# Optimization experiments

Hardware: AMD Instinct MI355X
Metric: run time of the kernel (lower is better)

Reference implementation:

```python
import jax, jax.numpy as jnp
import numpy as np

N_NODES = 500_000
N_FEAT = 16
HIDDEN = 32
N_EDGES = 8_000_000


def setup_inputs() -> dict:
    key = jax.random.key(0)
    ks = jax.random.split(key, 12)
    x = jax.random.normal(ks[0], (N_NODES, N_FEAT), dtype=jnp.float32)
    edge_index = jax.random.randint(ks[1], (2, N_EDGES), 0, N_NODES, dtype=jnp.int32)
    edge_weight = jax.random.uniform(ks[2], (N_EDGES,), dtype=jnp.float32)
    h = 0.1 * jax.random.normal(ks[3], (N_NODES, HIDDEN), dtype=jnp.float32)
    c = 0.1 * jax.random.normal(ks[4], (N_NODES, HIDDEN), dtype=jnp.float32)
    s = 0.1  # glorot-ish scale
    # Gate order along axis 0: (i, f, c~, o). K=1 ChebConv == Linear.
    W_x = s * jax.random.normal(ks[5], (4, N_FEAT, HIDDEN), dtype=jnp.float32)
    b_x = s * jax.random.normal(ks[6], (4, HIDDEN), dtype=jnp.float32)
    W_h = s * jax.random.normal(ks[7], (4, HIDDEN, HIDDEN), dtype=jnp.float32)
    b_h = s * jax.random.normal(ks[8], (4, HIDDEN), dtype=jnp.float32)
    w_c = s * jax.random.normal(ks[9], (3, HIDDEN), dtype=jnp.float32)  # peephole (i, f, o)
    b_g = s * jax.random.normal(ks[10], (4, HIDDEN), dtype=jnp.float32)  # per-gate bias b_i,b_f,b_c,b_o
    W_lin = s * jax.random.normal(ks[11], (HIDDEN, 1), dtype=jnp.float32)
    b_lin = jnp.zeros((1,), dtype=jnp.float32)
    return {"x": x, "edge_index": edge_index, "edge_weight": edge_weight,
            "h": h, "c": c, "W_x": W_x, "b_x": b_x, "W_h": W_h, "b_h": b_h,
            "w_c": w_c, "b_g": b_g, "W_lin": W_lin, "b_lin": b_lin}


def reference(x, edge_index, edge_weight, h, c, W_x, b_x, W_h, b_h, w_c, b_g, W_lin, b_lin):
    # GConvLSTM with K=1: each ChebConv degenerates to a single linear map
    # (Tx_0 = x, out = x @ W_0 + b); edge_index / edge_weight are unused by the math.
    # gx, gh: [4, N, H] — stacked (i, f, c~, o) gate pre-activations.
    gx = jnp.einsum('nf,gfh->gnh', x, W_x) + b_x[:, None, :]
    gh = jnp.einsum('nh,gho->gno', h, W_h) + b_h[:, None, :]
    s = gx + gh
    i = jax.nn.sigmoid(s[0] + w_c[0] * c + b_g[0])
    f = jax.nn.sigmoid(s[1] + w_c[1] * c + b_g[1])
    t = jnp.tanh(s[2] + b_g[2])
    c_new = f * c + i * t
    o = jax.nn.sigmoid(s[3] + w_c[2] * c_new + b_g[3])
    h0 = o * jnp.tanh(c_new)
    out = jax.nn.relu(h0) @ W_lin + b_lin  # [N, 1]
    return (out, h0, c_new)
```

## Files before the change

kernel.cpp:

```cpp
#include <hip/hip_runtime.h>
#include <hip/hip_bf16.h>

#define NF 16
#define NH 32
#define LOG2E  1.44269504088896340736f
#define TILE_NODES 32

#define T_WORDS 2560
#define XW 0
#define HW 512
#define CW 1536
#define HOUT 0
#define COUT 1152

typedef short bf16x8 __attribute__((ext_vector_type(8)));
typedef float f32x16 __attribute__((ext_vector_type(16)));
typedef float f32x4  __attribute__((ext_vector_type(4)));

#if __has_builtin(__builtin_amdgcn_exp2f)
#define EXP2(x) __builtin_amdgcn_exp2f(x)
#else
#define EXP2(x) exp2f(x)
#endif

__device__ __forceinline__ short f2bf(float f) {
    __hip_bfloat16 b = __float2bfloat16(f);
    return *reinterpret_cast<short*>(&b);
}

__device__ __forceinline__ bf16x8 cvt8(float4 a, float4 b) {
    bf16x8 r;
    r[0] = f2bf(a.x); r[1] = f2bf(a.y); r[2] = f2bf(a.z); r[3] = f2bf(a.w);
    r[4] = f2bf(b.x); r[5] = f2bf(b.y); r[6] = f2bf(b.z); r[7] = f2bf(b.w);
    return r;
}

__device__ __forceinline__ float sig2(float v) {
    return __builtin_amdgcn_rcpf(1.0f + EXP2(-v));
}
__device__ __forceinline__ float tanh2(float v) {
    return 1.0f - 2.0f * __builtin_amdgcn_rcpf(1.0f + EXP2(v));
}

__device__ __forceinline__ void gload_lds16(const float* g, float* l) {
    __builtin_amdgcn_global_load_lds(
        (const __attribute__((address_space(1))) void*)g,
        (__attribute__((address_space(3))) void*)l, 16, 0, 0);
}

__device__ __forceinline__ void nt_store4(float* p, float4 v) {
    f32x4 w = { v.x, v.y, v.z, v.w };
    __builtin_nontemporal_store(w, (f32x4*)p);
}

struct Frags { bf16x8 w[4][4]; bf16x8 a3; };

__global__ void prep_kernel(const float* __restrict__ Wx, const float* __restrict__ Wh,
                            const float* __restrict__ bx, const float* __restrict__ bh,
                            const float* __restrict__ bg, const float* __restrict__ wc,
                            short* __restrict__ Wpack, float* __restrict__ wcs)
{
    int t = blockIdx.x * blockDim.x + threadIdx.x;
    if (t < 4 * 4 * 64) {
        int g  = t >> 8;
        int ks = (t >> 6) & 3;
        int l  = t & 63;
        int col  = l & 31;
        int half = l >> 5;
        float scale = (g == 2) ? 2.0f * LOG2E : LOG2E;
        #pragma unroll
        for (int e = 0; e < 8; ++e) {
            int gk = ks * 16 + half * 8 + e;
            float w;
            if (gk < NF)            w = Wx[(g * NF + gk) * NH + col];
            else if (gk < NF + NH)  w = Wh[(g * NH + (gk - NF)) * NH + col];
            else if (gk == 48)      w = bx[g * NH + col] + bh[g * NH + col] + bg[g * NH + col];
            else                    w = 0.0f;
            Wpack[t * 8 + e] = f2bf(w * scale);
        }
    }
    if (t < 3 * NH) wcs[t] = wc[t] * LOG2E;
}

__device__ __forceinline__ void prefetch_tile(const float* __restrict__ x,
                                              const float* __restrict__ hin,
                                              const float* __restrict__ cin,
                                              long nb, float* ws,
                                              const int* xoff, const int* hoff)
{
    asm volatile("" ::: "memory");
    const float* xb = x   + nb * NF;
    const float* hb = hin + nb * NH;
    const float* cb = cin + nb * NH;
    #pragma unroll
    for (int i = 0; i < 2; ++i) gload_lds16(xb + xoff[i], ws + XW + i * 256);
    #pragma unroll
    for (int i = 0; i < 4; ++i) gload_lds16(hb + hoff[i], ws + HW + i * 256);
    #pragma unroll
    for (int i = 0; i < 4; ++i) gload_lds16(cb + hoff[i], ws + CW + i * 256);
    asm volatile("" ::: "memory");
}

__device__ __forceinline__ void do_tile(float* ws, long nb, const Frags& F,
                                        const float* __restrict__ wcs,
                                        const float* __restrict__ Wlin, float bl,
                                        float* __restrict__ out,
                                        float* __restrict__ h0o,
                                        float* __restrict__ co, int lane)
{
    const int col  = lane & 31;
    const int half = lane >> 5;
    const int c3 = col & 3, c7 = col & 7;

    float4 x0 = *(const float4*)&ws[XW + (col * 4 + ((2 * half)     ^ c3)) * 4];
    float4 x1 = *(const float4*)&ws[XW + (col * 4 + ((2 * half + 1) ^ c3)) * 4];
    float4 h0 = *(const float4*)&ws[HW + (col * 8 + ((2 * half)     ^ c7)) * 4];
    float4 h1 = *(const float4*)&ws[HW + (col * 8 + ((2 * half + 1) ^ c7)) * 4];
    float4 h2 = *(const float4*)&ws[HW + (col * 8 + ((4 + 2 * half) ^ c7)) * 4];
    float4 h3 = *(const float4*)&ws[HW + (col * 8 + ((5 + 2 * half) ^ c7)) * 4];
    bf16x8 a0 = cvt8(x0, x1), a1 = cvt8(h0, h1), a2 = cvt8(h2, h3);

    float4 cv4[4];
    #pragma unroll
    for (int jg = 0; jg < 4; ++jg)
        cv4[jg] = *(const float4*)&ws[CW + (col * 8 + ((2 * jg + half) ^ c7)) * 4];

    f32x16 acc[4];
    #pragma unroll
    for (int g = 0; g < 4; ++g) {
        #pragma unroll
        for (int r = 0; r < 16; ++r) acc[g][r] = 0.0f;
        acc[g] = __builtin_amdgcn_mfma_f32_32x32x16_bf16(F.w[g][0], a0,   acc[g], 0, 0, 0);
        acc[g] = __builtin_amdgcn_mfma_f32_32x32x16_bf16(F.w[g][1], a1,   acc[g], 0, 0, 0);
        acc[g] = __builtin_amdgcn_mfma_f32_32x32x16_bf16(F.w[g][2], a2,   acc[g], 0, 0, 0);
        acc[g] = __builtin_amdgcn_mfma_f32_32x32x16_bf16(F.w[g][3], F.a3, acc[g], 0, 0, 0);
    }

    float outacc = 0.0f;
    const float c2l = 2.0f * LOG2E;
    #pragma unroll
    for (int jg = 0; jg < 4; ++jg) {
        const int jbase = jg * 8 + 4 * half;
        const float4 w0 = *(const float4*)(wcs + 0 * NH + jbase);
        const float4 w1 = *(const float4*)(wcs + 1 * NH + jbase);
        const float4 w2 = *(const float4*)(wcs + 2 * NH + jbase);
        const float4 wl = *(const float4*)(Wlin + jbase);
        float h4[4], c4[4];
        #pragma unroll
        for (int q = 0; q < 4; ++q) {
            const int r = jg * 4 + q;
            const float ci = ((const float*)&cv4[jg])[q];
            const float ig = sig2(fmaf(((const float*)&w0)[q], ci, acc[0][r]));
            const float fg = sig2(fmaf(((const float*)&w1)[q], ci, acc[1][r]));
            const float tg = tanh2(acc[2][r]);
            const float cn = fg * ci + ig * tg;
            const float og = sig2(fmaf(((const float*)&w2)[q], cn, acc[3][r]));
            const float hh = og * tanh2(cn * c2l);
            c4[q] = cn;
            h4[q] = hh;
            outacc = fmaf(fmaxf(hh, 0.0f), ((const float*)&wl)[q], outacc);
        }
        *(float4*)&ws[HOUT + col * 36 + jbase] = make_float4(h4[0], h4[1], h4[2], h4[3]);
        *(float4*)&ws[COUT + col * 36 + jbase] = make_float4(c4[0], c4[1], c4[2], c4[3]);
    }

    float* hrow = h0o + nb * NH;
    float* crow = co  + nb * NH;
    #pragma unroll
    for (int rep = 0; rep < 4; ++rep) {
        const int tt = lane + rep * 64;
        const int nd = tt >> 3, j4 = (tt & 7) * 4;
        float4 vh = *(const float4*)&ws[HOUT + nd * 36 + j4];
        float4 vc = *(const float4*)&ws[COUT + nd * 36 + j4];
        nt_store4(hrow + tt * 4, vh);
        nt_store4(crow + tt * 4, vc);
    }

    outacc += __shfl_xor(outacc, 32, 64);
    if (half == 0) __builtin_nontemporal_store(outacc + bl, &out[nb + col]);
}

__global__ __launch_bounds__(256, 2) void lstm_pipe_kernel(
    const float* __restrict__ x, const float* __restrict__ hin,
    const float* __restrict__ cin,
    const float* __restrict__ Wlin, const float* __restrict__ blin,
    const short* __restrict__ Wpack, const float* __restrict__ wcs,
    float* __restrict__ out, float* __restrict__ h0o, float* __restrict__ co,
    int ntiles, int wstride)
{
    __shared__ float bufA[4][T_WORDS];
    __shared__ float bufB[4][T_WORDS];

    const int lane = threadIdx.x & 63;
    const int wave = threadIdx.x >> 6;
    float* cur = bufA[wave];
    float* oth = bufB[wave];

    Frags F;
    #pragma unroll
    for (int g = 0; g < 4; ++g)
        #pragma unroll
        for (int ks = 0; ks < 4; ++ks)
            F.w[g][ks] = *(const bf16x8*)(Wpack + (((g * 4) + ks) * 64 + lane) * 8);
    #pragma unroll
    for (int e = 0; e < 8; ++e) F.a3[e] = 0;
    if ((lane >> 5) == 0) F.a3[0] = (short)0x3F80;
    const float bl = blin[0];

    int xoff[2], hoff[4];
    #pragma unroll
    for (int i = 0; i < 2; ++i) {
        int u = i * 64 + lane;
        xoff[i] = ((u & ~3) | ((u & 3) ^ ((u >> 2) & 3))) * 4;
    }
    #pragma unroll
    for (int i = 0; i < 4; ++i) {
        int u = i * 64 + lane;
        hoff[i] = ((u & ~7) | ((u & 7) ^ ((u >> 3) & 7))) * 4;
    }

    const int S = wstride;
    const int last = ntiles - 1;
    int t = blockIdx.x * 4 + wave;

    prefetch_tile(x, hin, cin, (long)t * TILE_NODES, cur, xoff, hoff);
    {
        int t1 = t + S; if (t1 > last) t1 = last;
        prefetch_tile(x, hin, cin, (long)t1 * TILE_NODES, oth, xoff, hoff);
    }

    bool first = true;
    for (;;) {
        if (first) { asm volatile("s_waitcnt vmcnt(10)" ::: "memory"); first = false; }
        else       { asm volatile("s_waitcnt vmcnt(19)" ::: "memory"); }

        do_tile(cur, (long)t * TILE_NODES, F, wcs, Wlin, bl, out, h0o, co, lane);

        int tn = t + 2 * S; if (tn > last) tn = last;
        prefetch_tile(x, hin, cin, (long)tn * TILE_NODES, cur, xoff, hoff);

        t += S;
        if (t >= ntiles) break;
        float* tmp = cur; cur = oth; oth = tmp;
    }
}

extern "C" void kernel_launch(void* const* d_in, const int* in_sizes, int n_in,
                              void* d_out, int out_size, void* d_ws, size_t ws_size,
                              hipStream_t stream) {
    const float* x    = (const float*)d_in[0];
    const float* h    = (const float*)d_in[3];
    const float* c    = (const float*)d_in[4];
    const float* Wx   = (const float*)d_in[5];
    const float* bx   = (const float*)d_in[6];
    const float* Wh   = (const float*)d_in[7];
    const float* bh   = (const float*)d_in[8];
    const float* wc   = (const float*)d_in[9];
    const float* bg   = (const float*)d_in[10];
    const float* Wlin = (const float*)d_in[11];
    const float* blin = (const float*)d_in[12];

    const int N = in_sizes[0] / NF;
    const int ntiles = N / TILE_NODES;

    float* out = (float*)d_out;
    float* h0o = out + N;
    float* co  = h0o + (size_t)N * NH;

    short* Wpack = (short*)d_ws;
    float* wcs   = (float*)((char*)d_ws + 4 * 4 * 64 * 8 * sizeof(short));

    prep_kernel<<<4, 256, 0, stream>>>(Wx, Wh, bx, bh, bg, wc, Wpack, wcs);

    const int grid = 512;
    const int wstride = grid * 4;
    lstm_pipe_kernel<<<grid, 256, 0, stream>>>(
        x, h, c, Wlin, blin, Wpack, wcs, out, h0o, co, ntiles, wstride);
}
```

Baseline: 58.18 us.

## Load cell state directly into registers and shrink LDS staging per wave

```diff
diff --git a/kernel.cpp b/kernel.cpp
--- a/kernel.cpp
+++ b/kernel.cpp
@@ -6,12 +6,11 @@
 #define LOG2E  1.44269504088896340736f
 #define TILE_NODES 32
 
-#define T_WORDS 2560
+#define IN_WORDS 1536
 #define XW 0
 #define HW 512
-#define CW 1536
-#define HOUT 0
-#define COUT 1152
+#define OSTG 33
+#define OSTG_WORDS (32 * OSTG)
 
 typedef short bf16x8 __attribute__((ext_vector_type(8)));
 typedef float f32x16 __attribute__((ext_vector_type(16)));
@@ -82,26 +81,29 @@
     if (t < 3 * NH) wcs[t] = wc[t] * LOG2E;
 }
 
-__device__ __forceinline__ void prefetch_tile(const float* __restrict__ x,
-                                              const float* __restrict__ hin,
-                                              const float* __restrict__ cin,
-                                              long nb, float* ws,
-                                              const int* xoff, const int* hoff)
+__device__ __forceinline__ void prefetch_in(const float* __restrict__ x,
+                                            const float* __restrict__ hin,
+                                            long nb, float* ws,
+                                            const int* xoff, const int* hoff)
 {
     asm volatile("" ::: "memory");
     const float* xb = x   + nb * NF;
     const float* hb = hin + nb * NH;
-    const float* cb = cin + nb * NH;
     #pragma unroll
     for (int i = 0; i < 2; ++i) gload_lds16(xb + xoff[i], ws + XW + i * 256);
     #pragma unroll
     for (int i = 0; i < 4; ++i) gload_lds16(hb + hoff[i], ws + HW + i * 256);
-    #pragma unroll
-    for (int i = 0; i < 4; ++i) gload_lds16(cb + hoff[i], ws + CW + i * 256);
     asm volatile("" ::: "memory");
 }
 
-__device__ __forceinline__ void do_tile(float* ws, long nb, const Frags& F,
+#define LOAD_C(cr, nb_) {                                                   \
+    const float* pc = cin + ((nb_) + col) * NH + 4 * half;                  \
+    cr[0] = *(const float4*)(pc);      cr[1] = *(const float4*)(pc + 8);    \
+    cr[2] = *(const float4*)(pc + 16); cr[3] = *(const float4*)(pc + 24);   \
+    asm volatile("" ::: "memory"); }
+
+__device__ __forceinline__ void do_tile(const float* ws, float* og, long nb,
+                                        const float4* cr, const Frags& F,
                                         const float* __restrict__ wcs,
                                         const float* __restrict__ Wlin, float bl,
                                         float* __restrict__ out,
@@ -120,11 +122,6 @@
     float4 h3 = *(const float4*)&ws[HW + (col * 8 + ((5 + 2 * half) ^ c7)) * 4];
     bf16x8 a0 = cvt8(x0, x1), a1 = cvt8(h0, h1), a2 = cvt8(h2, h3);
 
-    float4 cv4[4];
-    #pragma unroll
-    for (int jg = 0; jg < 4; ++jg)
-        cv4[jg] = *(const float4*)&ws[CW + (col * 8 + ((2 * jg + half) ^ c7)) * 4];
-
     f32x16 acc[4];
     #pragma unroll
     for (int g = 0; g < 4; ++g) {
@@ -138,6 +135,7 @@
 
     float outacc = 0.0f;
     const float c2l = 2.0f * LOG2E;
+    float c4s0[4], c4s1[4], c4s2[4], c4s3[4];
     #pragma unroll
     for (int jg = 0; jg < 4; ++jg) {
         const int jbase = jg * 8 + 4 * half;
@@ -145,36 +143,51 @@
         const float4 w1 = *(const float4*)(wcs + 1 * NH + jbase);
         const float4 w2 = *(const float4*)(wcs + 2 * NH + jbase);
         const float4 wl = *(const float4*)(Wlin + jbase);
-        float h4[4], c4[4];
+        float h4[4];
         #pragma unroll
         for (int q = 0; q < 4; ++q) {
             const int r = jg * 4 + q;
-            const float ci = ((const float*)&cv4[jg])[q];
+            const float ci = ((const float*)&cr[jg])[q];
             const float ig = sig2(fmaf(((const float*)&w0)[q], ci, acc[0][r]));
             const float fg = sig2(fmaf(((const float*)&w1)[q], ci, acc[1][r]));
             const float tg = tanh2(acc[2][r]);
             const float cn = fg * ci + ig * tg;
-            const float og = sig2(fmaf(((const float*)&w2)[q], cn, acc[3][r]));
-            const float hh = og * tanh2(cn * c2l);
-            c4[q] = cn;
+            const float og_ = sig2(fmaf(((const float*)&w2)[q], cn, acc[3][r]));
+            const float hh = og_ * tanh2(cn * c2l);
+            if (jg == 0) c4s0[q] = cn; else if (jg == 1) c4s1[q] = cn;
+            else if (jg == 2) c4s2[q] = cn; else c4s3[q] = cn;
             h4[q] = hh;
             outacc = fmaf(fmaxf(hh, 0.0f), ((const float*)&wl)[q], outacc);
         }
-        *(float4*)&ws[HOUT + col * 36 + jbase] = make_float4(h4[0], h4[1], h4[2], h4[3]);
-        *(float4*)&ws[COUT + col * 36 + jbase] = make_float4(c4[0], c4[1], c4[2], c4[3]);
+        *(float4*)&og[col * OSTG + jbase] = make_float4(h4[0], h4[1], h4[2], h4[3]);
     }
 
     float* hrow = h0o + nb * NH;
     float* crow = co  + nb * NH;
+    float4 vh[4];
     #pragma unroll
     for (int rep = 0; rep < 4; ++rep) {
         const int tt = lane + rep * 64;
-        const int nd = tt >> 3, j4 = (tt & 7) * 4;
-        float4 vh = *(const float4*)&ws[HOUT + nd * 36 + j4];
-        float4 vc = *(const float4*)&ws[COUT + nd * 36 + j4];
-        nt_store4(hrow + tt * 4, vh);
-        nt_store4(crow + tt * 4, vc);
-    }
+        vh[rep] = *(const float4*)&og[(tt >> 3) * OSTG + (tt & 7) * 4];
+    }
+    #pragma unroll
+    for (int rep = 0; rep < 4; ++rep) nt_store4(hrow + (lane + rep * 64) * 4, vh[rep]);
+
+    {
+        const int jb0 = 4 * half;
+        *(float4*)&og[col * OSTG + jb0]      = make_float4(c4s0[0], c4s0[1], c4s0[2], c4s0[3]);
+        *(float4*)&og[col * OSTG + jb0 + 8]  = make_float4(c4s1[0], c4s1[1], c4s1[2], c4s1[3]);
+        *(float4*)&og[col * OSTG + jb0 + 16] = make_float4(c4s2[0], c4s2[1], c4s2[2], c4s2[3]);
+        *(float4*)&og[col * OSTG + jb0 + 24] = make_float4(c4s3[0], c4s3[1], c4s3[2], c4s3[3]);
+    }
+    float4 vc[4];
+    #pragma unroll
+    for (int rep = 0; rep < 4; ++rep) {
+        const int tt = lane + rep * 64;
+        vc[rep] = *(const float4*)&og[(tt >> 3) * OSTG + (tt & 7) * 4];
+    }
+    #pragma unroll
+    for (int rep = 0; rep < 4; ++rep) nt_store4(crow + (lane + rep * 64) * 4, vc[rep]);
 
     outacc += __shfl_xor(outacc, 32, 64);
     if (half == 0) __builtin_nontemporal_store(outacc + bl, &out[nb + col]);
@@ -188,13 +201,17 @@
     float* __restrict__ out, float* __restrict__ h0o, float* __restrict__ co,
     int ntiles, int wstride)
 {
-    __shared__ float bufA[4][T_WORDS];
-    __shared__ float bufB[4][T_WORDS];
+    __shared__ float bufA[4][IN_WORDS];
+    __shared__ float bufB[4][IN_WORDS];
+    __shared__ float ostg[4][OSTG_WORDS];
 
     const int lane = threadIdx.x & 63;
     const int wave = threadIdx.x >> 6;
-    float* cur = bufA[wave];
-    float* oth = bufB[wave];
+    const int col  = lane & 31;
+    const int half = lane >> 5;
+    float* wsA = bufA[wave];
+    float* wsB = bufB[wave];
+    float* og  = ostg[wave];
 
     Frags F;
     #pragma unroll
@@ -204,7 +221,7 @@
             F.w[g][ks] = *(const bf16x8*)(Wpack + (((g * 4) + ks) * 64 + lane) * 8);
     #pragma unroll
     for (int e = 0; e < 8; ++e) F.a3[e] = 0;
-    if ((lane >> 5) == 0) F.a3[0] = (short)0x3F80;
+    if (half == 0) F.a3[0] = (short)0x3F80;
     const float bl = blin[0];
 
     int xoff[2], hoff[4];
@@ -223,25 +240,38 @@
     const int last = ntiles - 1;
     int t = blockIdx.x * 4 + wave;
 
-    prefetch_tile(x, hin, cin, (long)t * TILE_NODES, cur, xoff, hoff);
+    float4 crA[4], crB[4];
+
+    prefetch_in(x, hin, (long)t * TILE_NODES, wsA, xoff, hoff);
+    LOAD_C(crA, (long)t * TILE_NODES);
+
     {
-        int t1 = t + S; if (t1 > last) t1 = last;
-        prefetch_tile(x, hin, cin, (long)t1 * TILE_NODES, oth, xoff, hoff);
-    }
-
-    bool first = true;
-    for (;;) {
-        if (first) { asm volatile("s_waitcnt vmcnt(10)" ::: "memory"); first = false; }
-        else       { asm volatile("s_waitcnt vmcnt(19)" ::: "memory"); }
-
-        do_tile(cur, (long)t * TILE_NODES, F, wcs, Wlin, bl, out, h0o, co, lane);
-
-        int tn = t + 2 * S; if (tn > last) tn = last;
-        prefetch_tile(x, hin, cin, (long)tn * TILE_NODES, cur, xoff, hoff);
-
+        asm volatile("s_waitcnt vmcnt(0)" ::: "memory");
+        int tn = t + S; if (tn > last) tn = last;
+        prefetch_in(x, hin, (long)tn * TILE_NODES, wsB, xoff, hoff);
+        LOAD_C(crB, (long)tn * TILE_NODES);
+        do_tile(wsA, og, (long)t * TILE_NODES, crA, F, wcs, Wlin, bl, out, h0o, co, lane);
         t += S;
-        if (t >= ntiles) break;
-        float* tmp = cur; cur = oth; oth = tmp;
+    }
+    if (t < ntiles) {
+        for (;;) {
+            asm volatile("s_waitcnt vmcnt(9)" ::: "memory");
+            {
+                int tn = t + S; if (tn > last) tn = last;
+                prefetch_in(x, hin, (long)tn * TILE_NODES, wsA, xoff, hoff);
+                LOAD_C(crA, (long)tn * TILE_NODES);
+                do_tile(wsB, og, (long)t * TILE_NODES, crB, F, wcs, Wlin, bl, out, h0o, co, lane);
+            }
+            t += S; if (t >= ntiles) break;
+            asm volatile("s_waitcnt vmcnt(9)" ::: "memory");
+            {
+                int tn = t + S; if (tn > last) tn = last;
+                prefetch_in(x, hin, (long)tn * TILE_NODES, wsB, xoff, hoff);
+                LOAD_C(crB, (long)tn * TILE_NODES);
+                do_tile(wsA, og, (long)t * TILE_NODES, crA, F, wcs, Wlin, bl, out, h0o, co, lane);
+            }
+            t += S; if (t >= ntiles) break;
+        }
     }
 }
 
```

Result: slower. 64.00 us (+10.0%).

## Load c directly to registers, shrink LDS staging, raise occupancy to 3 blocks

Applied to the files above, without the earlier changes.

```diff
diff --git a/kernel.cpp b/kernel.cpp
--- a/kernel.cpp
+++ b/kernel.cpp
@@ -4,14 +4,13 @@
 #define NF 16
 #define NH 32
 #define LOG2E  1.44269504088896340736f
-#define TILE_NODES 32
-
-#define T_WORDS 2560
+#define TILE 32
+
+#define IN_WORDS 1536
 #define XW 0
 #define HW 512
-#define CW 1536
-#define HOUT 0
-#define COUT 1152
+#define OSTG 33
+#define OSTG_WORDS (32 * OSTG)
 
 typedef short bf16x8 __attribute__((ext_vector_type(8)));
 typedef float f32x16 __attribute__((ext_vector_type(16)));
@@ -82,26 +81,29 @@
     if (t < 3 * NH) wcs[t] = wc[t] * LOG2E;
 }
 
-__device__ __forceinline__ void prefetch_tile(const float* __restrict__ x,
-                                              const float* __restrict__ hin,
-                                              const float* __restrict__ cin,
-                                              long nb, float* ws,
-                                              const int* xoff, const int* hoff)
+__device__ __forceinline__ void prefetch_xh(const float* __restrict__ x,
+                                            const float* __restrict__ hin,
+                                            long nb, float* ws,
+                                            const int* xoff, const int* hoff)
 {
     asm volatile("" ::: "memory");
     const float* xb = x   + nb * NF;
     const float* hb = hin + nb * NH;
-    const float* cb = cin + nb * NH;
     #pragma unroll
     for (int i = 0; i < 2; ++i) gload_lds16(xb + xoff[i], ws + XW + i * 256);
     #pragma unroll
     for (int i = 0; i < 4; ++i) gload_lds16(hb + hoff[i], ws + HW + i * 256);
-    #pragma unroll
-    for (int i = 0; i < 4; ++i) gload_lds16(cb + hoff[i], ws + CW + i * 256);
     asm volatile("" ::: "memory");
 }
 
-__device__ __forceinline__ void do_tile(float* ws, long nb, const Frags& F,
+#define LOAD_C(cr, t_) {                                                     \
+    const float* pc = cin + ((long)(t_) * TILE + col) * NH + 4 * half;       \
+    cr[0] = *(const float4*)(pc);      cr[1] = *(const float4*)(pc + 8);     \
+    cr[2] = *(const float4*)(pc + 16); cr[3] = *(const float4*)(pc + 24);    \
+    asm volatile("" ::: "memory"); }
+
+__device__ __forceinline__ void do_tile(float* ws, long nb,
+                                        const float4* cr, const Frags& F,
                                         const float* __restrict__ wcs,
                                         const float* __restrict__ Wlin, float bl,
                                         float* __restrict__ out,
@@ -120,11 +122,6 @@
     float4 h3 = *(const float4*)&ws[HW + (col * 8 + ((5 + 2 * half) ^ c7)) * 4];
     bf16x8 a0 = cvt8(x0, x1), a1 = cvt8(h0, h1), a2 = cvt8(h2, h3);
 
-    float4 cv4[4];
-    #pragma unroll
-    for (int jg = 0; jg < 4; ++jg)
-        cv4[jg] = *(const float4*)&ws[CW + (col * 8 + ((2 * jg + half) ^ c7)) * 4];
-
     f32x16 acc[4];
     #pragma unroll
     for (int g = 0; g < 4; ++g) {
@@ -138,6 +135,7 @@
 
     float outacc = 0.0f;
     const float c2l = 2.0f * LOG2E;
+    float c4s0[4], c4s1[4], c4s2[4], c4s3[4];
     #pragma unroll
     for (int jg = 0; jg < 4; ++jg) {
         const int jbase = jg * 8 + 4 * half;
@@ -145,23 +143,23 @@
         const float4 w1 = *(const float4*)(wcs + 1 * NH + jbase);
         const float4 w2 = *(const float4*)(wcs + 2 * NH + jbase);
         const float4 wl = *(const float4*)(Wlin + jbase);
-        float h4[4], c4[4];
+        float h4[4];
         #pragma unroll
         for (int q = 0; q < 4; ++q) {
             const int r = jg * 4 + q;
-            const float ci = ((const float*)&cv4[jg])[q];
+            const float ci = ((const float*)&cr[jg])[q];
             const float ig = sig2(fmaf(((const float*)&w0)[q], ci, acc[0][r]));
             const float fg = sig2(fmaf(((const float*)&w1)[q], ci, acc[1][r]));
             const float tg = tanh2(acc[2][r]);
             const float cn = fg * ci + ig * tg;
             const float og = sig2(fmaf(((const float*)&w2)[q], cn, acc[3][r]));
             const float hh = og * tanh2(cn * c2l);
-            c4[q] = cn;
+            if (jg == 0) c4s0[q] = cn; else if (jg == 1) c4s1[q] = cn;
+            else if (jg == 2) c4s2[q] = cn; else c4s3[q] = cn;
             h4[q] = hh;
             outacc = fmaf(fmaxf(hh, 0.0f), ((const float*)&wl)[q], outacc);
         }
-        *(float4*)&ws[HOUT + col * 36 + jbase] = make_float4(h4[0], h4[1], h4[2], h4[3]);
-        *(float4*)&ws[COUT + col * 36 + jbase] = make_float4(c4[0], c4[1], c4[2], c4[3]);
+        *(float4*)&ws[col * OSTG + jbase] = make_float4(h4[0], h4[1], h4[2], h4[3]);
     }
 
     float* hrow = h0o + nb * NH;
@@ -169,10 +167,21 @@
     #pragma unroll
     for (int rep = 0; rep < 4; ++rep) {
         const int tt = lane + rep * 64;
-        const int nd = tt >> 3, j4 = (tt & 7) * 4;
-        float4 vh = *(const float4*)&ws[HOUT + nd * 36 + j4];
-        float4 vc = *(const float4*)&ws[COUT + nd * 36 + j4];
+        float4 vh = *(const float4*)&ws[(tt >> 3) * OSTG + (tt & 7) * 4];
         nt_store4(hrow + tt * 4, vh);
+    }
+
+    {
+        const int jb0 = 4 * half;
+        *(float4*)&ws[col * OSTG + jb0]      = make_float4(c4s0[0], c4s0[1], c4s0[2], c4s0[3]);
+        *(float4*)&ws[col * OSTG + jb0 + 8]  = make_float4(c4s1[0], c4s1[1], c4s1[2], c4s1[3]);
+        *(float4*)&ws[col * OSTG + jb0 + 16] = make_float4(c4s2[0], c4s2[1], c4s2[2], c4s2[3]);
+        *(float4*)&ws[col * OSTG + jb0 + 24] = make_float4(c4s3[0], c4s3[1], c4s3[2], c4s3[3]);
+    }
+    #pragma unroll
+    for (int rep = 0; rep < 4; ++rep) {
+        const int tt = lane + rep * 64;
+        float4 vc = *(const float4*)&ws[(tt >> 3) * OSTG + (tt & 7) * 4];
         nt_store4(crow + tt * 4, vc);
     }
 
@@ -180,7 +189,7 @@
     if (half == 0) __builtin_nontemporal_store(outacc + bl, &out[nb + col]);
 }
 
-__global__ __launch_bounds__(256, 2) void lstm_pipe_kernel(
+__global__ __launch_bounds__(256, 3) void lstm_pipe_kernel(
     const float* __restrict__ x, const float* __restrict__ hin,
     const float* __restrict__ cin,
     const float* __restrict__ Wlin, const float* __restrict__ blin,
@@ -188,11 +197,13 @@
     float* __restrict__ out, float* __restrict__ h0o, float* __restrict__ co,
     int ntiles, int wstride)
 {
-    __shared__ float bufA[4][T_WORDS];
-    __shared__ float bufB[4][T_WORDS];
+    __shared__ float bufA[4][IN_WORDS];
+    __shared__ float bufB[4][IN_WORDS];
 
     const int lane = threadIdx.x & 63;
     const int wave = threadIdx.x >> 6;
+    const int col  = lane & 31;
+    const int half = lane >> 5;
     float* cur = bufA[wave];
     float* oth = bufB[wave];
 
@@ -204,7 +215,7 @@
             F.w[g][ks] = *(const bf16x8*)(Wpack + (((g * 4) + ks) * 64 + lane) * 8);
     #pragma unroll
     for (int e = 0; e < 8; ++e) F.a3[e] = 0;
-    if ((lane >> 5) == 0) F.a3[0] = (short)0x3F80;
+    if (half == 0) F.a3[0] = (short)0x3F80;
     const float bl = blin[0];
 
     int xoff[2], hoff[4];
@@ -223,21 +234,28 @@
     const int last = ntiles - 1;
     int t = blockIdx.x * 4 + wave;
 
-    prefetch_tile(x, hin, cin, (long)t * TILE_NODES, cur, xoff, hoff);
+    float4 crA[4], crB[4];
+
+    prefetch_xh(x, hin, (long)t * TILE, cur, xoff, hoff);
+    LOAD_C(crA, t);
     {
         int t1 = t + S; if (t1 > last) t1 = last;
-        prefetch_tile(x, hin, cin, (long)t1 * TILE_NODES, oth, xoff, hoff);
+        prefetch_xh(x, hin, (long)t1 * TILE, oth, xoff, hoff);
+        LOAD_C(crB, t1);
     }
 
     bool first = true;
     for (;;) {
-        if (first) { asm volatile("s_waitcnt vmcnt(10)" ::: "memory"); first = false; }
-        else       { asm volatile("s_waitcnt vmcnt(19)" ::: "memory"); }
-
-        do_tile(cur, (long)t * TILE_NODES, F, wcs, Wlin, bl, out, h0o, co, lane);
+        if (first) { asm volatile("s_waitcnt vmcnt(14)" ::: "memory"); first = false; }
+        else       { asm volatile("s_waitcnt vmcnt(23)" ::: "memory"); }
+
+        do_tile(cur, (long)t * TILE,
+                ((t / S) & 1) ? crB : crA,
+                F, wcs, Wlin, bl, out, h0o, co, lane);
 
         int tn = t + 2 * S; if (tn > last) tn = last;
-        prefetch_tile(x, hin, cin, (long)tn * TILE_NODES, cur, xoff, hoff);
+        prefetch_xh(x, hin, (long)tn * TILE, cur, xoff, hoff);
+        if (((t / S) & 1) == 0) { LOAD_C(crA, tn); } else { LOAD_C(crB, tn); }
 
         t += S;
         if (t >= ntiles) break;
@@ -261,7 +279,7 @@
     const float* blin = (const float*)d_in[12];
 
     const int N = in_sizes[0] / NF;
-    const int ntiles = N / TILE_NODES;
+    const int ntiles = N / TILE;
 
     float* out = (float*)d_out;
     float* h0o = out + N;
@@ -272,7 +290,7 @@
 
     prep_kernel<<<4, 256, 0, stream>>>(Wx, Wh, bx, bh, bg, wc, Wpack, wcs);
 
-    const int grid = 512;
+    const int grid = 768;
     const int wstride = grid * 4;
     lstm_pipe_kernel<<<grid, 256, 0, stream>>>(
         x, h, c, Wlin, blin, Wpack, wcs, out, h0o, co, ntiles, wstride);
```

New measurement: 121.3 us. 108% more time.
